# Kernel tuning notes

Hardware: AMD Instinct MI355X
Metric: run time of the kernel (lower is better)

The kernel has to match this reference:

```python
import jax, jax.numpy as jnp
import numpy as np

B, N, M = 64, 1024, 1024
MAX_ITER = 10      # init default max_iter
EPS = 1e-4         # init default epsilon


def setup_inputs() -> dict:
    key = jax.random.key(0)
    k1, k2, k3 = jax.random.split(key, 3)
    s = jax.random.uniform(k1, (B, N, M), dtype=jnp.float32)
    # ragged valid sizes per batch element, in [N//2, N]
    nrows = jax.random.randint(k2, (B,), N // 2, N + 1, dtype=jnp.int32)
    ncols = jax.random.randint(k3, (B,), M // 2, M + 1, dtype=jnp.int32)
    return {"s": s, "nrows": nrows, "ncols": ncols}


def reference(s, nrows, ncols):
    # Faithful vectorized form of the torch loop:
    #   even iter: sum[b,i,j] = sum_{k<nrows[b]} s[b,k,j]  (masked column sums)
    #   odd  iter: sum[b,i,j] = sum_{k<ncols[b]} s[b,i,k]  (masked row sums)
    #   then s[b,i,j] *= 1/sum inside the [nrows[b], ncols[b]] block, 0 outside.
    Bb, Nn, Mm = s.shape
    row_mask = jnp.arange(Nn)[None, :] < nrows[:, None]          # [B, N]
    col_mask = jnp.arange(Mm)[None, :] < ncols[:, None]          # [B, M]
    block = row_mask[:, :, None] & col_mask[:, None, :]          # [B, N, M]

    s = s + jnp.float32(EPS)
    for i in range(MAX_ITER):
        if i % 2 == 0:
            # column normalization: sum over valid rows
            d = jnp.sum(jnp.where(row_mask[:, :, None], s, 0.0), axis=1, keepdims=True)  # [B,1,M]
            d = jnp.where(col_mask[:, None, :], d, 1.0)  # safe denom outside block
        else:
            # row normalization: sum over valid cols
            d = jnp.sum(jnp.where(col_mask[:, None, :], s, 0.0), axis=2, keepdims=True)  # [B,N,1]
            d = jnp.where(row_mask[:, :, None], d, 1.0)
        s = jnp.where(block, s / d, 0.0)
    return s
```

## Files before the change

### kernel.cpp

```cpp
#include <hip/hip_runtime.h>


#define BB 64
#define NN 1024
#define MM 1024
#define EPS 1e-4f

typedef _Float16 half_t;
typedef __attribute__((ext_vector_type(4))) _Float16 half4_t;
typedef __attribute__((ext_vector_type(8))) _Float16 half8_t;
typedef __attribute__((ext_vector_type(4))) float float4_t;
typedef __attribute__((ext_vector_type(2))) float float2_t;

__global__ __launch_bounds__(256) void prep_kernel(
    const float* __restrict__ s, const int* __restrict__ nrows,
    const int* __restrict__ ncols, half_t* __restrict__ H,
    float* __restrict__ P) {
  int b = blockIdx.z, rc = blockIdx.y, stripe = blockIdx.x;
  int nr = nrows[b], nc = ncols[b];
  float* Pp = P + ((size_t)rc * BB + b) * MM + stripe * 128;
  if (stripe * 128 >= nc) {
    if (threadIdx.x < 128) Pp[threadIdx.x] = 0.f;
    return;
  }
  int tc = threadIdx.x & 31, tr = threadIdx.x >> 5;
  int j0 = stripe * 128 + tc * 4;
  const float* sp = s + (size_t)b * NN * MM + j0;
  half_t* hp = H + (size_t)b * NN * MM + j0;
  float4_t acc = {0.f, 0.f, 0.f, 0.f};
  int base = rc * 128;
#pragma unroll
  for (int it = 0; it < 16; it++) {
    int i = base + it * 8 + tr;
    if (i < nr) {
      float4_t v = *(const float4_t*)(sp + (size_t)i * MM);
      v.x += EPS; v.y += EPS; v.z += EPS; v.w += EPS;
      half4_t h = {(half_t)v.x, (half_t)v.y, (half_t)v.z, (half_t)v.w};
      *(half4_t*)(hp + (size_t)i * MM) = h;
      acc.x += v.x; acc.y += v.y; acc.z += v.z; acc.w += v.w;
    }
  }
  __shared__ float lds[8][128];
  *(float4_t*)&lds[tr][tc * 4] = acc;
  __syncthreads();
  if (threadIdx.x < 128) {
    float s0 = 0.f;
#pragma unroll
    for (int k = 0; k < 8; k++) s0 += lds[k][threadIdx.x];
    Pp[threadIdx.x] = s0;
  }
}

__global__ __launch_bounds__(256) void creduce_kernel(
    const float* __restrict__ P, const int* __restrict__ ncols,
    float* __restrict__ C) {
  int b = blockIdx.y;
  int j = blockIdx.x * 256 + threadIdx.x;
  int nc = ncols[b];
  float s0 = 0.f;
#pragma unroll
  for (int k = 0; k < 8; k++) s0 += P[((size_t)k * BB + b) * MM + j];
  C[b * MM + j] = (j < nc) ? 1.f / s0 : 0.f;
}

__global__ __launch_bounds__(512) void fused_kernel(
    const half_t* __restrict__ H, const int* __restrict__ nrows,
    const int* __restrict__ ncols, const float* __restrict__ C,
    float* __restrict__ P) {
  int b = blockIdx.y, ch = blockIdx.x;
  int nr = nrows[b], nc = ncols[b];
  int l = threadIdx.x & 63, w = threadIdx.x >> 6;
  const float* Cp = C + b * MM;
  float c0[8], c1[8];
  *(float4_t*)&c0[0] = *(const float4_t*)(Cp + l * 8);
  *(float4_t*)&c0[4] = *(const float4_t*)(Cp + l * 8 + 4);
  *(float4_t*)&c1[0] = *(const float4_t*)(Cp + 512 + l * 8);
  *(float4_t*)&c1[4] = *(const float4_t*)(Cp + 512 + l * 8 + 4);
  bool hi = (512 + l * 8) < nc;
  const half_t* hp = H + (size_t)b * NN * MM + l * 8;
  float a0[8] = {0.f, 0.f, 0.f, 0.f, 0.f, 0.f, 0.f, 0.f};
  float a1[8] = {0.f, 0.f, 0.f, 0.f, 0.f, 0.f, 0.f, 0.f};
  int rbase = ch * 128 + w;
#pragma unroll 4
  for (int r = 0; r < 16; r++) {
    int i = rbase + (r << 3);
    if (i < nr) {
      const half_t* hr = hp + (size_t)i * MM;
      half8_t h0 = *(const half8_t*)hr;
      float f0[8];
#pragma unroll
      for (int k = 0; k < 8; k++) f0[k] = (float)h0[k];
      float acc = f0[0] * c0[0] + f0[1] * c0[1] + f0[2] * c0[2] +
                  f0[3] * c0[3] + f0[4] * c0[4] + f0[5] * c0[5] +
                  f0[6] * c0[6] + f0[7] * c0[7];
      float f1[8];
      if (hi) {
        half8_t h1 = *(const half8_t*)(hr + 512);
#pragma unroll
        for (int k = 0; k < 8; k++) f1[k] = (float)h1[k];
        acc += f1[0] * c1[0] + f1[1] * c1[1] + f1[2] * c1[2] +
               f1[3] * c1[3] + f1[4] * c1[4] + f1[5] * c1[5] +
               f1[6] * c1[6] + f1[7] * c1[7];
      }
#pragma unroll
      for (int off = 32; off > 0; off >>= 1) acc += __shfl_xor(acc, off, 64);
      float rv = 1.f / acc;
#pragma unroll
      for (int k = 0; k < 8; k++) a0[k] += f0[k] * rv;
      if (hi) {
#pragma unroll
        for (int k = 0; k < 8; k++) a1[k] += f1[k] * rv;
      }
    }
  }
  __shared__ float lds[8][MM];
#pragma unroll
  for (int k = 0; k < 8; k++) lds[w][l * 8 + k] = a0[k];
#pragma unroll
  for (int k = 0; k < 8; k++) lds[w][512 + l * 8 + k] = a1[k];
  __syncthreads();
  int t = threadIdx.x;
  float s0 = 0.f, s1 = 0.f;
#pragma unroll
  for (int k = 0; k < 8; k++) {
    s0 += lds[k][t * 2];
    s1 += lds[k][t * 2 + 1];
  }
  float2_t o = {s0, s1};
  *(float2_t*)(P + ((size_t)ch * BB + b) * MM + t * 2) = o;
}

__global__ __launch_bounds__(256) void final_kernel(
    const float* __restrict__ s, const int* __restrict__ nrows,
    const int* __restrict__ ncols, const float* __restrict__ C,
    float* __restrict__ out) {
  int b = blockIdx.y;
  int nr = nrows[b], nc = ncols[b];
  int w = threadIdx.x >> 6, l = threadIdx.x & 63;
  int i = blockIdx.x * 4 + w;
  float* op = out + ((size_t)b * NN + i) * MM;
  float4_t z = {0.f, 0.f, 0.f, 0.f};
  if (i >= nr) {
#pragma unroll
    for (int ch = 0; ch < 4; ch++) *(float4_t*)(op + ch * 256 + l * 4) = z;
    return;
  }
  const float* sp = s + ((size_t)b * NN + i) * MM;
  const float* Cp = C + b * MM;
  float4_t sv[4], cv[4];
  float acc = 0.f;
  int nch = (nc + 255) >> 8;
#pragma unroll
  for (int ch = 0; ch < 4; ch++) {
    if (ch < nch) {
      float4_t v = *(const float4_t*)(sp + ch * 256 + l * 4);
      v.x += EPS; v.y += EPS; v.z += EPS; v.w += EPS;
      sv[ch] = v;
      float4_t c = *(const float4_t*)(Cp + ch * 256 + l * 4);
      cv[ch] = c;
      acc += v.x * c.x + v.y * c.y + v.z * c.z + v.w * c.w;
    }
  }
#pragma unroll
  for (int off = 32; off > 0; off >>= 1) acc += __shfl_xor(acc, off, 64);
  float r = 1.f / acc;
#pragma unroll
  for (int ch = 0; ch < 4; ch++) {
    if (ch < nch) {
      float4_t o;
      o.x = sv[ch].x * cv[ch].x * r;
      o.y = sv[ch].y * cv[ch].y * r;
      o.z = sv[ch].z * cv[ch].z * r;
      o.w = sv[ch].w * cv[ch].w * r;
      *(float4_t*)(op + ch * 256 + l * 4) = o;
    } else {
      *(float4_t*)(op + ch * 256 + l * 4) = z;
    }
  }
}

extern "C" void kernel_launch(void* const* d_in, const int* in_sizes, int n_in,
                              void* d_out, int out_size, void* d_ws,
                              size_t ws_size, hipStream_t stream) {
  const float* s = (const float*)d_in[0];
  const int* nrows = (const int*)d_in[1];
  const int* ncols = (const int*)d_in[2];
  float* out = (float*)d_out;
  half_t* H = (half_t*)d_out;
  float* C = (float*)d_ws;
  float* P = C + BB * MM;

  dim3 pgrid(8, 8, BB);
  dim3 dgrid(4, BB);
  dim3 ugrid(8, BB);
  dim3 fgrid(NN / 4, BB);

  prep_kernel<<<pgrid, 256, 0, stream>>>(s, nrows, ncols, H, P);
  creduce_kernel<<<dgrid, 256, 0, stream>>>(P, ncols, C);
  for (int t = 0; t < 4; t++) {
    fused_kernel<<<ugrid, 512, 0, stream>>>(H, nrows, ncols, C, P);
    creduce_kernel<<<dgrid, 256, 0, stream>>>(P, ncols, C);
  }
  final_kernel<<<fgrid, 256, 0, stream>>>(s, nrows, ncols, C, out);
}
```

Measured before the change: 566.4 us.

## Fuse Sinkhorn pipeline into one cooperative persistent kernel with grid syncs

Replaces the chain of prep, column-reduce, four fused passes and final kernels with a single cooperative kernel. The kernel keeps each block resident and uses grid.sync between phases, ping-ponging partial column sums between two workspace buffers. It folds the column reciprocals into LDS inside each block, so the separate creduce launches disappear. This removes roughly ten kernel launches and their gaps. In exchange, the final normalisation pass now runs on only 512 blocks instead of a very wide grid, which could lower memory-level parallelism. If the cooperative launch fails, the code falls back to the old multi-kernel path.

```diff
diff --git a/kernel.cpp b/kernel.cpp
--- a/kernel.cpp
+++ b/kernel.cpp
@@ -1,4 +1,7 @@
 #include <hip/hip_runtime.h>
+#include <hip/hip_cooperative_groups.h>
+
+namespace cg = cooperative_groups;
 
 
 #define BB 64
@@ -11,6 +14,225 @@
 typedef __attribute__((ext_vector_type(8))) _Float16 half8_t;
 typedef __attribute__((ext_vector_type(4))) float float4_t;
 typedef __attribute__((ext_vector_type(2))) float float2_t;
+
+__device__ __forceinline__ void foldC(const float* __restrict__ Pc,
+                                      float* cld, int b, int nc, int t) {
+  float s0 = 0.f, s1 = 0.f;
+#pragma unroll
+  for (int k = 0; k < 8; k++) {
+    float2_t p = *(const float2_t*)(Pc + ((size_t)k * BB + b) * MM + t * 2);
+    s0 += p.x;
+    s1 += p.y;
+  }
+  cld[t * 2] = (t * 2 < nc) ? 1.f / s0 : 0.f;
+  cld[t * 2 + 1] = (t * 2 + 1 < nc) ? 1.f / s1 : 0.f;
+}
+
+__device__ __forceinline__ void colReduceStore(float (&red)[8][MM],
+                                               const float* a0,
+                                               const float* a1, int w, int l,
+                                               int t, float* Pdst) {
+#pragma unroll
+  for (int k = 0; k < 8; k++) red[w][l * 8 + k] = a0[k];
+#pragma unroll
+  for (int k = 0; k < 8; k++) red[w][512 + l * 8 + k] = a1[k];
+  __syncthreads();
+  float s0 = 0.f, s1 = 0.f;
+#pragma unroll
+  for (int k = 0; k < 8; k++) {
+    s0 += red[k][t * 2];
+    s1 += red[k][t * 2 + 1];
+  }
+  float2_t o = {s0, s1};
+  *(float2_t*)(Pdst + t * 2) = o;
+}
+
+__global__ __launch_bounds__(512, 4) void sink_coop(
+    const float* __restrict__ s, const int* __restrict__ nrows,
+    const int* __restrict__ ncols, float* __restrict__ out,
+    float* __restrict__ Pa, float* __restrict__ Pb) {
+  cg::grid_group grid = cg::this_grid();
+  const int bid = blockIdx.x;
+  const int b = bid & (BB - 1), ch = bid >> 6;
+  const int nr = nrows[b], nc = ncols[b];
+  const int t = threadIdx.x;
+  const int l = t & 63, w = t >> 6;
+
+  __shared__ float red[8][MM];
+  __shared__ float cld[MM];
+
+  half_t* H = (half_t*)out;
+  const size_t mat = (size_t)b * NN * MM;
+  const bool hi = (512 + l * 8) < nc;
+  const int rbase = ch * 128 + w;
+  float* Pme_a = Pa + ((size_t)ch * BB + b) * MM;
+  float* Pme_b = Pb + ((size_t)ch * BB + b) * MM;
+
+  {
+    float a0[8] = {0.f, 0.f, 0.f, 0.f, 0.f, 0.f, 0.f, 0.f};
+    float a1[8] = {0.f, 0.f, 0.f, 0.f, 0.f, 0.f, 0.f, 0.f};
+    const float* sp = s + mat + l * 8;
+    half_t* hp = H + mat + l * 8;
+#pragma unroll 4
+    for (int r = 0; r < 16; r++) {
+      int i = rbase + (r << 3);
+      if (i < nr) {
+        const float* srow = sp + (size_t)i * MM;
+        half_t* hrow = hp + (size_t)i * MM;
+        float f0[8], f1[8];
+        {
+          float4_t u = *(const float4_t*)srow;
+          float4_t v = *(const float4_t*)(srow + 4);
+          f0[0] = u.x + EPS; f0[1] = u.y + EPS; f0[2] = u.z + EPS;
+          f0[3] = u.w + EPS; f0[4] = v.x + EPS; f0[5] = v.y + EPS;
+          f0[6] = v.z + EPS; f0[7] = v.w + EPS;
+        }
+        {
+          float4_t u = *(const float4_t*)(srow + 512);
+          float4_t v = *(const float4_t*)(srow + 516);
+          f1[0] = u.x + EPS; f1[1] = u.y + EPS; f1[2] = u.z + EPS;
+          f1[3] = u.w + EPS; f1[4] = v.x + EPS; f1[5] = v.y + EPS;
+          f1[6] = v.z + EPS; f1[7] = v.w + EPS;
+        }
+        half8_t h0, h1;
+#pragma unroll
+        for (int k = 0; k < 8; k++) h0[k] = (half_t)f0[k];
+#pragma unroll
+        for (int k = 0; k < 8; k++) h1[k] = (half_t)f1[k];
+        *(half8_t*)hrow = h0;
+        *(half8_t*)(hrow + 512) = h1;
+#pragma unroll
+        for (int k = 0; k < 8; k++) a0[k] += f0[k];
+#pragma unroll
+        for (int k = 0; k < 8; k++) a1[k] += f1[k];
+      }
+    }
+    colReduceStore(red, a0, a1, w, l, t, Pme_a);
+  }
+  grid.sync();
+
+  float* Pc = Pa;
+  float* Pme_n = Pme_b;
+  float* Pme_c = Pme_a;
+  for (int pass = 0; pass < 4; pass++) {
+    foldC(Pc, cld, b, nc, t);
+    __syncthreads();
+    float c0[8], c1[8];
+#pragma unroll
+    for (int k = 0; k < 8; k++) c0[k] = cld[l * 8 + k];
+#pragma unroll
+    for (int k = 0; k < 8; k++) c1[k] = cld[512 + l * 8 + k];
+    float a0[8] = {0.f, 0.f, 0.f, 0.f, 0.f, 0.f, 0.f, 0.f};
+    float a1[8] = {0.f, 0.f, 0.f, 0.f, 0.f, 0.f, 0.f, 0.f};
+    const half_t* hp = H + mat + l * 8;
+#pragma unroll 4
+    for (int r = 0; r < 16; r++) {
+      int i = rbase + (r << 3);
+      if (i < nr) {
+        const half_t* hr = hp + (size_t)i * MM;
+        half8_t h0 = *(const half8_t*)hr;
+        float f0[8];
+#pragma unroll
+        for (int k = 0; k < 8; k++) f0[k] = (float)h0[k];
+        float acc = f0[0] * c0[0] + f0[1] * c0[1] + f0[2] * c0[2] +
+                    f0[3] * c0[3] + f0[4] * c0[4] + f0[5] * c0[5] +
+                    f0[6] * c0[6] + f0[7] * c0[7];
+        float f1[8];
+        if (hi) {
+          half8_t h1 = *(const half8_t*)(hr + 512);
+#pragma unroll
+          for (int k = 0; k < 8; k++) f1[k] = (float)h1[k];
+          acc += f1[0] * c1[0] + f1[1] * c1[1] + f1[2] * c1[2] +
+                 f1[3] * c1[3] + f1[4] * c1[4] + f1[5] * c1[5] +
+                 f1[6] * c1[6] + f1[7] * c1[7];
+        }
+#pragma unroll
+        for (int off = 32; off > 0; off >>= 1)
+          acc += __shfl_xor(acc, off, 64);
+        float rv = 1.f / acc;
+#pragma unroll
+        for (int k = 0; k < 8; k++) a0[k] += f0[k] * rv;
+        if (hi) {
+#pragma unroll
+          for (int k = 0; k < 8; k++) a1[k] += f1[k] * rv;
+        }
+      }
+    }
+    colReduceStore(red, a0, a1, w, l, t, Pme_n);
+    grid.sync();
+    Pc = (pass & 1) ? Pa : Pb;
+    float* tmp = Pme_n; Pme_n = Pme_c; Pme_c = tmp;
+  }
+
+  foldC(Pc, cld, b, nc, t);
+  __syncthreads();
+  {
+    float c0[8], c1[8];
+#pragma unroll
+    for (int k = 0; k < 8; k++) c0[k] = cld[l * 8 + k];
+#pragma unroll
+    for (int k = 0; k < 8; k++) c1[k] = cld[512 + l * 8 + k];
+    const float* sp = s + mat + l * 8;
+    float* op = out + mat + l * 8;
+    float4_t z = {0.f, 0.f, 0.f, 0.f};
+#pragma unroll 2
+    for (int r = 0; r < 16; r++) {
+      int i = rbase + (r << 3);
+      float* orow = op + (size_t)i * MM;
+      if (i >= nr) {
+        *(float4_t*)orow = z;
+        *(float4_t*)(orow + 4) = z;
+        *(float4_t*)(orow + 512) = z;
+        *(float4_t*)(orow + 516) = z;
+        continue;
+      }
+      const float* srow = sp + (size_t)i * MM;
+      float f0[8], f1[8];
+      {
+        float4_t u = *(const float4_t*)srow;
+        float4_t v = *(const float4_t*)(srow + 4);
+        f0[0] = u.x + EPS; f0[1] = u.y + EPS; f0[2] = u.z + EPS;
+        f0[3] = u.w + EPS; f0[4] = v.x + EPS; f0[5] = v.y + EPS;
+        f0[6] = v.z + EPS; f0[7] = v.w + EPS;
+      }
+      float acc = f0[0] * c0[0] + f0[1] * c0[1] + f0[2] * c0[2] +
+                  f0[3] * c0[3] + f0[4] * c0[4] + f0[5] * c0[5] +
+                  f0[6] * c0[6] + f0[7] * c0[7];
+      if (hi) {
+        float4_t u = *(const float4_t*)(srow + 512);
+        float4_t v = *(const float4_t*)(srow + 516);
+        f1[0] = u.x + EPS; f1[1] = u.y + EPS; f1[2] = u.z + EPS;
+        f1[3] = u.w + EPS; f1[4] = v.x + EPS; f1[5] = v.y + EPS;
+        f1[6] = v.z + EPS; f1[7] = v.w + EPS;
+        acc += f1[0] * c1[0] + f1[1] * c1[1] + f1[2] * c1[2] +
+               f1[3] * c1[3] + f1[4] * c1[4] + f1[5] * c1[5] +
+               f1[6] * c1[6] + f1[7] * c1[7];
+      }
+#pragma unroll
+      for (int off = 32; off > 0; off >>= 1) acc += __shfl_xor(acc, off, 64);
+      float rv = 1.f / acc;
+      float4_t o;
+      o.x = f0[0] * c0[0] * rv; o.y = f0[1] * c0[1] * rv;
+      o.z = f0[2] * c0[2] * rv; o.w = f0[3] * c0[3] * rv;
+      *(float4_t*)orow = o;
+      o.x = f0[4] * c0[4] * rv; o.y = f0[5] * c0[5] * rv;
+      o.z = f0[6] * c0[6] * rv; o.w = f0[7] * c0[7] * rv;
+      *(float4_t*)(orow + 4) = o;
+      if (hi) {
+        o.x = f1[0] * c1[0] * rv; o.y = f1[1] * c1[1] * rv;
+        o.z = f1[2] * c1[2] * rv; o.w = f1[3] * c1[3] * rv;
+        *(float4_t*)(orow + 512) = o;
+        o.x = f1[4] * c1[4] * rv; o.y = f1[5] * c1[5] * rv;
+        o.z = f1[6] * c1[6] * rv; o.w = f1[7] * c1[7] * rv;
+        *(float4_t*)(orow + 516) = o;
+      } else {
+        *(float4_t*)(orow + 512) = z;
+        *(float4_t*)(orow + 516) = z;
+      }
+    }
+  }
+}
+
 
 __global__ __launch_bounds__(256) void prep_kernel(
     const float* __restrict__ s, const int* __restrict__ nrows,
@@ -186,20 +408,27 @@
   const int* nrows = (const int*)d_in[1];
   const int* ncols = (const int*)d_in[2];
   float* out = (float*)d_out;
-  half_t* H = (half_t*)d_out;
-  float* C = (float*)d_ws;
-  float* P = C + BB * MM;
-
-  dim3 pgrid(8, 8, BB);
-  dim3 dgrid(4, BB);
-  dim3 ugrid(8, BB);
-  dim3 fgrid(NN / 4, BB);
-
-  prep_kernel<<<pgrid, 256, 0, stream>>>(s, nrows, ncols, H, P);
-  creduce_kernel<<<dgrid, 256, 0, stream>>>(P, ncols, C);
-  for (int t = 0; t < 4; t++) {
-    fused_kernel<<<ugrid, 512, 0, stream>>>(H, nrows, ncols, C, P);
+  float* Pa = (float*)d_ws;
+  float* Pb = Pa + 8 * BB * MM;
+  float* C = Pb + 8 * BB * MM;
+
+  void* args[] = {(void*)&s, (void*)&nrows, (void*)&ncols,
+                  (void*)&out, (void*)&Pa, (void*)&Pb};
+  hipError_t err = hipLaunchCooperativeKernel(sink_coop, dim3(512), dim3(512),
+                                              args, 0, stream);
+  if (err != hipSuccess) {
+    half_t* H = (half_t*)d_out;
+    float* P = Pa;
+    dim3 pgrid(8, 8, BB);
+    dim3 dgrid(4, BB);
+    dim3 ugrid(8, BB);
+    dim3 fgrid(NN / 4, BB);
+    prep_kernel<<<pgrid, 256, 0, stream>>>(s, nrows, ncols, H, P);
     creduce_kernel<<<dgrid, 256, 0, stream>>>(P, ncols, C);
-  }
-  final_kernel<<<fgrid, 256, 0, stream>>>(s, nrows, ncols, C, out);
-}
+    for (int t = 0; t < 4; t++) {
+      fused_kernel<<<ugrid, 512, 0, stream>>>(H, nrows, ncols, C, P);
+      creduce_kernel<<<dgrid, 256, 0, stream>>>(P, ncols, C);
+    }
+    final_kernel<<<fgrid, 256, 0, stream>>>(s, nrows, ncols, C, out);
+  }
+}
```

Result: slower. 874.2 us (+54.3%).
